# Performance work log

Measured on AMD Instinct MI355X. Metric: run time of the kernel, lower is better.

The kernel has to match this reference:

```python
import jax, jax.numpy as jnp
import numpy as np

N_NODES = 50000
N_EDGES = 600000
D = 128


def _mean_agg(h, src, dst, n_nodes):
    # DGL SAGEConv 'mean': mean of incoming src features per dst node; 0 for isolated nodes
    s = jax.ops.segment_sum(h[src], dst, num_segments=n_nodes)  # [N, d]
    deg = jax.ops.segment_sum(jnp.ones_like(dst, dtype=h.dtype), dst, num_segments=n_nodes)
    return s / jnp.maximum(deg, 1.0)[:, None]


def setup_inputs() -> dict:
    key = jax.random.key(0)
    ks = jax.random.split(key, 10)
    sc = 1.0 / np.sqrt(D)
    return {
        "x": jax.random.normal(ks[0], (N_NODES, D), jnp.float32),
        "e": jax.random.normal(ks[1], (N_EDGES, D), jnp.float32),
        "src": jax.random.randint(ks[2], (N_EDGES,), 0, N_NODES, jnp.int32),
        "dst": jax.random.randint(ks[3], (N_EDGES,), 0, N_NODES, jnp.int32),
        "W1_self": jax.random.normal(ks[4], (D, D), jnp.float32) * sc,
        "W1_neigh": jax.random.normal(ks[5], (D, D), jnp.float32) * sc,
        "b1": jnp.zeros((D,), jnp.float32),
        "W2_self": jax.random.normal(ks[6], (D, D), jnp.float32) * sc,
        "W2_neigh": jax.random.normal(ks[7], (D, D), jnp.float32) * sc,
        "b2": jnp.zeros((D,), jnp.float32),
        "Wp": jax.random.normal(ks[8], (2 * D, 3), jnp.float32) * (1.0 / np.sqrt(2 * D)),
        "bp": jnp.zeros((3,), jnp.float32),
    }


def reference(x, e, src, dst, W1_self, W1_neigh, b1, W2_self, W2_neigh, b2, Wp, bp):
    n = x.shape[0]
    # SAGEConv 1 (mean) + ReLU
    agg1 = _mean_agg(x, src, dst, n)
    h = jax.nn.relu(x @ W1_self + agg1 @ W1_neigh + b1)
    # SAGEConv 2 (mean)
    agg2 = _mean_agg(h, src, dst, n)
    h = h @ W2_self + agg2 @ W2_neigh + b2
    # MLPPredictor: per-edge gather, concat, linear (edge feature e unused in score)
    he = jnp.concatenate([h[src], h[dst]], axis=1)  # [E, 2D]
    score = he @ Wp + bp  # [E, 3]
    return score
```

## Files before the change

### kernel.cpp

```cpp
#include <hip/hip_runtime.h>
#include <hip/hip_bf16.h>


typedef __attribute__((ext_vector_type(8))) short bf16x8;
typedef __attribute__((ext_vector_type(4))) float f32x4;
typedef __attribute__((ext_vector_type(2))) float f32x2;

#if defined(__has_builtin)
#if __has_builtin(__builtin_amdgcn_cvt_pk_f32_fp8)
#define USE_FP8_GATHER 1
#endif
#endif
#ifndef USE_FP8_GATHER
#define USE_FP8_GATHER 0
#endif

static __device__ __forceinline__ float bf16lo(unsigned u) {
    return __uint_as_float(u << 16);
}
static __device__ __forceinline__ float bf16hi(unsigned u) {
    return __uint_as_float(u & 0xffff0000u);
}
static __device__ __forceinline__ unsigned short f2bf(float f) {
    unsigned u = __float_as_uint(f);
    unsigned r = 0x7fffu + ((u >> 16) & 1u);
    return (unsigned short)((u + r) >> 16);
}
static __device__ __forceinline__ unsigned pack_bf162(float a, float b) {
    return (unsigned)f2bf(a) | ((unsigned)f2bf(b) << 16);
}

static __device__ __forceinline__ unsigned f2fp8(float f) {
    unsigned b = __float_as_uint(f);
    unsigned s = (b >> 24) & 0x80u;
    float af = fabsf(f);
    unsigned code;
    if (af < 0.015625f) {
        code = (unsigned)rintf(af * 512.f);
    } else {
        unsigned u = (b & 0x7FFFFFFFu) + 0x7FFFFu + ((b >> 20) & 1u);
        unsigned e = (u >> 23) - 120u;
        code = (e << 3) | ((u >> 20) & 7u);
    }
    return s | code;
}

#define SORT_BLOCKS 128

__global__ __launch_bounds__(256) void k_misc(
    const float* __restrict__ x, unsigned short* __restrict__ xb,
    unsigned char* __restrict__ xq,
    const int* __restrict__ dst, int* __restrict__ H,
    const float* __restrict__ W1s, const float* __restrict__ W1n,
    unsigned short* __restrict__ Wt1,
    const float* __restrict__ W2s, const float* __restrict__ W2n,
    const float* __restrict__ Wp, const float* __restrict__ b2,
    const float* __restrict__ bp, float* __restrict__ Wc,
    float* __restrict__ bconst, int N, int E, int CHUNK)
{
    const int nCvt = (N * 32 + 255) / 256;
    const int b = blockIdx.x;
    const int t = threadIdx.x;

    if (b < nCvt) {
        int i = b * 256 + t;
        if (i < N * 32) {
            float4 v = ((const float4*)x)[i];
            uint2 o;
            o.x = pack_bf162(v.x, v.y);
            o.y = pack_bf162(v.z, v.w);
            *(uint2*)(xb + (size_t)i * 4) = o;
            unsigned q = f2fp8(v.x) | (f2fp8(v.y) << 8) |
                         (f2fp8(v.z) << 16) | (f2fp8(v.w) << 24);
            *(unsigned*)(xq + (size_t)i * 4) = q;
        }
    } else if (b < nCvt + SORT_BLOCKS) {
        __shared__ int hist[256];
        hist[t] = 0;
        __syncthreads();
        int blk = b - nCvt;
        int start = blk * CHUNK;
        int end = min(start + CHUNK, E);
        for (int e = start + t; e < end; e += 256)
            atomicAdd(&hist[((unsigned)dst[e]) >> 8], 1);
        __syncthreads();
        H[blk * 256 + t] = hist[t];
    } else if (b < nCvt + SORT_BLOCKS + 128) {
        int id = (b - nCvt - SORT_BLOCKS) * 256 + t;
        int k = id >> 7, n = id & 127;
        float v;
        if (k < 128) {
            v = W1s[k * 128 + n];
        } else {
#if USE_FP8_GATHER
            int K = k - 128;
            int ksb = K >> 5, r = K & 31, lkp = r >> 3, i = r & 7;
            int orig = lkp * 32 + ksb * 8 + i;
            v = W1n[orig * 128 + n];
#else
            v = W1n[(k - 128) * 128 + n];
#endif
        }
        Wt1[n * 256 + k] = f2bf(v);
    } else {
        for (int id = t; id < 1539; id += 256) {
            if (id < 1536) {
                int c = id / 12, j = id % 12;
                int q = j / 3, jj = j % 3;
                const float* W2 = (q == 0 || q == 2) ? W2s : W2n;
                int wpoff = (q < 2) ? 0 : 128;
                float s = 0.f;
                for (int m = 0; m < 128; ++m)
                    s += W2[c * 128 + m] * Wp[(wpoff + m) * 3 + jj];
                Wc[c * 12 + j] = s;
            } else {
                int jj = id - 1536;
                float s = bp[jj];
                for (int m = 0; m < 128; ++m)
                    s += b2[m] * (Wp[m * 3 + jj] + Wp[(128 + m) * 3 + jj]);
                bconst[jj] = s;
            }
        }
    }
}

__global__ __launch_bounds__(256) void k_s3(const int* __restrict__ src,
                                            const int* __restrict__ dst,
                                            const int* __restrict__ H,
                                            int* __restrict__ packed,
                                            int* __restrict__ bucketBase,
                                            int E, int CHUNK) {
    __shared__ int lt[256];
    __shared__ int cur[256];
    const int t = threadIdx.x, blk = blockIdx.x;
    int tot = 0, pre = 0;
    for (int b = 0; b < SORT_BLOCKS; ++b) {
        int h = H[b * 256 + t];
        pre += (b < blk) ? h : 0;
        tot += h;
    }
    lt[t] = tot;
    __syncthreads();
    for (int off = 1; off < 256; off <<= 1) {
        int u = (t >= off) ? lt[t - off] : 0;
        __syncthreads();
        lt[t] += u;
        __syncthreads();
    }
    int excl = lt[t] - tot;
    cur[t] = excl + pre;
    if (blk == 0) {
        bucketBase[t] = excl;
        if (t == 0) bucketBase[256] = E;
    }
    __syncthreads();
    int start = blk * CHUNK, end = min(start + CHUNK, E);
    for (int e = start + t; e < end; e += 256) {
        int d = dst[e];
        int p = atomicAdd(&cur[((unsigned)d) >> 8], 1);
        packed[p] = (src[e] & 0xFFFF) | ((d & 255) << 16);
    }
}

__global__ __launch_bounds__(256) void k_s4(const int* __restrict__ packed,
                                            const int* __restrict__ bucketBase,
                                            int* __restrict__ eidx,
                                            int* __restrict__ cursor,
                                            float* __restrict__ fdeg,
                                            float* __restrict__ invdeg, int N) {
    const int t = threadIdx.x, b = blockIdx.x;
    const int rb = bucketBase[b], re = bucketBase[b + 1];
    __shared__ int cnt[256];
    __shared__ int lt[256];
    __shared__ int cur[256];
    cnt[t] = 0;
    __syncthreads();
    for (int i = rb + t; i < re; i += 256)
        atomicAdd(&cnt[(packed[i] >> 16) & 255], 1);
    __syncthreads();
    int v = cnt[t];
    lt[t] = v;
    __syncthreads();
    for (int off = 1; off < 256; off <<= 1) {
        int u = (t >= off) ? lt[t - off] : 0;
        __syncthreads();
        lt[t] += u;
        __syncthreads();
    }
    int excl = lt[t] - v;
    int node = b * 256 + t;
    if (node < N) {
        cursor[node] = rb + excl + v;
        fdeg[node] = (float)v;
        invdeg[node] = 1.0f / fmaxf((float)v, 1.0f);
    }
    cur[t] = rb + excl;
    __syncthreads();
    for (int i = rb + t; i < re; i += 256) {
        int p = packed[i];
        int pos = atomicAdd(&cur[(p >> 16) & 255], 1);
        eidx[pos] = p & 0xFFFF;
    }
}

__global__ __launch_bounds__(256) void k_gemm_fused(
    const unsigned short* __restrict__ xb,
    const unsigned char* __restrict__ xq,
    const int* __restrict__ eidx, const int* __restrict__ cursor,
    const float* __restrict__ fdeg, const float* __restrict__ invdeg,
    const unsigned short* __restrict__ Wt, const float* __restrict__ bias,
    const float* __restrict__ Wc, float* __restrict__ P, int N)
{
    __shared__ __align__(16) char sW[65536];
    __shared__ float sWc[1536];
    const int t = threadIdx.x;
    const int wave = t >> 6, lane = t & 63;
    const int lrow = lane & 15, lk = lane >> 4;
    const int r0 = blockIdx.x * 64 + wave * 16 + lrow;

    int* eidxL = (int*)sW;
    const int nb0 = blockIdx.x * 64;
    const int lastN = min(nb0 + 63, N - 1);
    const int estart = cursor[nb0] - (int)fdeg[nb0];
    const int eend = cursor[lastN];
    const int ecnt = eend - estart;
    const bool ldsOK = (ecnt <= 16384);
    if (ldsOK) {
        for (int i = t; i < ecnt; i += 256) eidxL[i] = eidx[estart + i];
    }
    __syncthreads();

    union { bf16x8 v; unsigned u[4]; } afrag0[4];

#if USE_FP8_GATHER
#define ACCQ(AGG, A, B)                                                      \
    {                                                                        \
        f32x2 p;                                                             \
        p = __builtin_amdgcn_cvt_pk_f32_fp8((int)(A).x, false);              \
        AGG[0][0] += p.x; AGG[0][1] += p.y;                                  \
        p = __builtin_amdgcn_cvt_pk_f32_fp8((int)(A).x, true);               \
        AGG[0][2] += p.x; AGG[0][3] += p.y;                                  \
        p = __builtin_amdgcn_cvt_pk_f32_fp8((int)(A).y, false);              \
        AGG[0][4] += p.x; AGG[0][5] += p.y;                                  \
        p = __builtin_amdgcn_cvt_pk_f32_fp8((int)(A).y, true);               \
        AGG[0][6] += p.x; AGG[0][7] += p.y;                                  \
        p = __builtin_amdgcn_cvt_pk_f32_fp8((int)(A).z, false);              \
        AGG[1][0] += p.x; AGG[1][1] += p.y;                                  \
        p = __builtin_amdgcn_cvt_pk_f32_fp8((int)(A).z, true);               \
        AGG[1][2] += p.x; AGG[1][3] += p.y;                                  \
        p = __builtin_amdgcn_cvt_pk_f32_fp8((int)(A).w, false);              \
        AGG[1][4] += p.x; AGG[1][5] += p.y;                                  \
        p = __builtin_amdgcn_cvt_pk_f32_fp8((int)(A).w, true);               \
        AGG[1][6] += p.x; AGG[1][7] += p.y;                                  \
        p = __builtin_amdgcn_cvt_pk_f32_fp8((int)(B).x, false);              \
        AGG[2][0] += p.x; AGG[2][1] += p.y;                                  \
        p = __builtin_amdgcn_cvt_pk_f32_fp8((int)(B).x, true);               \
        AGG[2][2] += p.x; AGG[2][3] += p.y;                                  \
        p = __builtin_amdgcn_cvt_pk_f32_fp8((int)(B).y, false);              \
        AGG[2][4] += p.x; AGG[2][5] += p.y;                                  \
        p = __builtin_amdgcn_cvt_pk_f32_fp8((int)(B).y, true);               \
        AGG[2][6] += p.x; AGG[2][7] += p.y;                                  \
        p = __builtin_amdgcn_cvt_pk_f32_fp8((int)(B).z, false);              \
        AGG[3][0] += p.x; AGG[3][1] += p.y;                                  \
        p = __builtin_amdgcn_cvt_pk_f32_fp8((int)(B).z, true);               \
        AGG[3][2] += p.x; AGG[3][3] += p.y;                                  \
        p = __builtin_amdgcn_cvt_pk_f32_fp8((int)(B).w, false);              \
        AGG[3][4] += p.x; AGG[3][5] += p.y;                                  \
        p = __builtin_amdgcn_cvt_pk_f32_fp8((int)(B).w, true);               \
        AGG[3][6] += p.x; AGG[3][7] += p.y;                                  \
    }
#endif

    {
        float agg[4][8];
#pragma unroll
        for (int k = 0; k < 4; ++k)
#pragma unroll
            for (int i = 0; i < 8; ++i) agg[k][i] = 0.f;

        if (r0 < N) {
            int d = (int)fdeg[r0];
            int o;
            const int* EP;
            if (ldsOK) { EP = eidxL; o = cursor[r0] - d - estart; }
            else       { EP = eidx;  o = cursor[r0] - d; }
            int j = 0;
#if USE_FP8_GATHER
            for (; j + 2 <= d; j += 2) {
                int s0 = EP[o + j], s1 = EP[o + j + 1];
                const unsigned char* row0 = xq + (size_t)s0 * 128 + lk * 32;
                const unsigned char* row1 = xq + (size_t)s1 * 128 + lk * 32;
                uint4 A0 = *(const uint4*)(row0);
                uint4 B0 = *(const uint4*)(row0 + 16);
                uint4 A1 = *(const uint4*)(row1);
                uint4 B1 = *(const uint4*)(row1 + 16);
                ACCQ(agg, A0, B0)
                ACCQ(agg, A1, B1)
            }
            if (j < d) {
                int s0 = EP[o + j];
                const unsigned char* row0 = xq + (size_t)s0 * 128 + lk * 32;
                uint4 A0 = *(const uint4*)(row0);
                uint4 B0 = *(const uint4*)(row0 + 16);
                ACCQ(agg, A0, B0)
            }
#else
            for (; j + 2 <= d; j += 2) {
                int s0 = EP[o + j], s1 = EP[o + j + 1];
                const unsigned short* row0 = xb + (size_t)s0 * 128 + lk * 8;
                const unsigned short* row1 = xb + (size_t)s1 * 128 + lk * 8;
                uint4 v0[4], v1[4];
#pragma unroll
                for (int k = 0; k < 4; ++k) {
                    v0[k] = *(const uint4*)(row0 + k * 32);
                    v1[k] = *(const uint4*)(row1 + k * 32);
                }
#pragma unroll
                for (int k = 0; k < 4; ++k) {
                    agg[k][0] += bf16lo(v0[k].x); agg[k][1] += bf16hi(v0[k].x);
                    agg[k][2] += bf16lo(v0[k].y); agg[k][3] += bf16hi(v0[k].y);
                    agg[k][4] += bf16lo(v0[k].z); agg[k][5] += bf16hi(v0[k].z);
                    agg[k][6] += bf16lo(v0[k].w); agg[k][7] += bf16hi(v0[k].w);
                    agg[k][0] += bf16lo(v1[k].x); agg[k][1] += bf16hi(v1[k].x);
                    agg[k][2] += bf16lo(v1[k].y); agg[k][3] += bf16hi(v1[k].y);
                    agg[k][4] += bf16lo(v1[k].z); agg[k][5] += bf16hi(v1[k].z);
                    agg[k][6] += bf16lo(v1[k].w); agg[k][7] += bf16hi(v1[k].w);
                }
            }
            if (j < d) {
                int s0 = EP[o + j];
                const unsigned short* row0 = xb + (size_t)s0 * 128 + lk * 8;
#pragma unroll
                for (int k = 0; k < 4; ++k) {
                    uint4 v0 = *(const uint4*)(row0 + k * 32);
                    agg[k][0] += bf16lo(v0.x); agg[k][1] += bf16hi(v0.x);
                    agg[k][2] += bf16lo(v0.y); agg[k][3] += bf16hi(v0.y);
                    agg[k][4] += bf16lo(v0.z); agg[k][5] += bf16hi(v0.z);
                    agg[k][6] += bf16lo(v0.w); agg[k][7] += bf16hi(v0.w);
                }
            }
#endif
            float sc = invdeg[r0];
#pragma unroll
            for (int k = 0; k < 4; ++k)
#pragma unroll
                for (int i = 0; i < 4; ++i)
                    afrag0[k].u[i] = pack_bf162(agg[k][2 * i] * sc,
                                                agg[k][2 * i + 1] * sc);
        } else {
#pragma unroll
            for (int k = 0; k < 4; ++k)
#pragma unroll
                for (int i = 0; i < 4; ++i) afrag0[k].u[i] = 0u;
        }
    }

    __syncthreads();
#pragma unroll
    for (int i = 0; i < 16; ++i) {
        int o = (i * 256 + t) * 16;
        int n = o >> 9;
        int c = o & 511;
        int sw = (n << 9) | (c ^ ((n & 7) << 4));
        *(float4*)&sW[sw] = *(const float4*)((const char*)Wt + o);
    }
    for (int i = t; i < 1536; i += 256) sWc[i] = Wc[i];

    f32x4 acc[8];
#pragma unroll
    for (int nb = 0; nb < 8; ++nb) acc[nb] = (f32x4){0.f, 0.f, 0.f, 0.f};

    __syncthreads();

    for (int ks = 0; ks < 8; ++ks) {
        bf16x8 a0;
        if (ks < 4) {
            const int kk = ks * 32 + lk * 8;
            a0 = (bf16x8){};
            if (r0 < N) a0 = *(const bf16x8*)(xb + (size_t)r0 * 128 + kk);
        } else {
            a0 = afrag0[ks - 4].v;
        }
        const int cbase = ks * 64 + lk * 16;
#pragma unroll
        for (int nb = 0; nb < 8; ++nb) {
            int n = nb * 16 + lrow;
            int sw = (n << 9) | (cbase ^ ((n & 7) << 4));
            bf16x8 b = *(const bf16x8*)&sW[sw];
            acc[nb] = __builtin_amdgcn_mfma_f32_16x16x32_bf16(a0, b, acc[nb], 0, 0, 0);
        }
    }

    {
        float hval[8][4];
#pragma unroll
        for (int nb = 0; nb < 8; ++nb) {
            float bv = bias[nb * 16 + lrow];
#pragma unroll
            for (int r = 0; r < 4; ++r)
                hval[nb][r] = fmaxf(acc[nb][r] + bv, 0.f);
        }
#pragma unroll
        for (int r = 0; r < 4; ++r) {
            float pj[12];
#pragma unroll
            for (int j = 0; j < 12; ++j) pj[j] = 0.f;
#pragma unroll
            for (int nb = 0; nb < 8; ++nb) {
                float hv = hval[nb][r];
                const float* wrow = &sWc[(nb * 16 + lrow) * 12];
#pragma unroll
                for (int j = 0; j < 12; ++j) pj[j] += hv * wrow[j];
            }
#pragma unroll
            for (int off = 8; off; off >>= 1) {
#pragma unroll
                for (int j = 0; j < 12; ++j) pj[j] += __shfl_xor(pj[j], off, 64);
            }
            int node = blockIdx.x * 64 + wave * 16 + lk * 4 + r;
            if (lrow == 0 && node < N) {
                float* prow = &P[(size_t)node * 16];
                *(float4*)(prow + 0)  = make_float4(pj[0], pj[1], pj[2], pj[6]);
                *(float4*)(prow + 4)  = make_float4(pj[7], pj[8], 0.f, 0.f);
                *(float4*)(prow + 8)  = make_float4(pj[3], pj[4], pj[5], pj[9]);
                *(float4*)(prow + 12) = make_float4(pj[10], pj[11], 0.f, 0.f);
            }
        }
    }
}

__global__ __launch_bounds__(256) void k_agg3(const float* __restrict__ P,
                                              const int* __restrict__ eidx,
                                              const int* __restrict__ cursor,
                                              const float* __restrict__ fdeg,
                                              const float* __restrict__ invdeg,
                                              float4* __restrict__ ps4,
                                              float4* __restrict__ pd4, int N) {
    int g = blockIdx.x * 256 + threadIdx.x;
    if (g >= N) return;
    int d = (int)fdeg[g];
    int o = cursor[g] - d;
    float a0 = 0.f, a1 = 0.f, a2 = 0.f, a3 = 0.f, a4 = 0.f, a5 = 0.f;
    int i = 0;
    for (; i + 2 <= d; i += 2) {
        int s0 = eidx[o + i], s1 = eidx[o + i + 1];
        float4 u0 = *(const float4*)&P[(size_t)s0 * 16 + 8];
        float4 u1 = *(const float4*)&P[(size_t)s0 * 16 + 12];
        float4 w0 = *(const float4*)&P[(size_t)s1 * 16 + 8];
        float4 w1 = *(const float4*)&P[(size_t)s1 * 16 + 12];
        a0 += u0.x; a1 += u0.y; a2 += u0.z; a3 += u0.w; a4 += u1.x; a5 += u1.y;
        a0 += w0.x; a1 += w0.y; a2 += w0.z; a3 += w0.w; a4 += w1.x; a5 += w1.y;
    }
    if (i < d) {
        int s0 = eidx[o + i];
        float4 u0 = *(const float4*)&P[(size_t)s0 * 16 + 8];
        float4 u1 = *(const float4*)&P[(size_t)s0 * 16 + 12];
        a0 += u0.x; a1 += u0.y; a2 += u0.z; a3 += u0.w; a4 += u1.x; a5 += u1.y;
    }
    float sc = invdeg[g];
    float4 s0v = *(const float4*)&P[(size_t)g * 16];
    float4 s1v = *(const float4*)&P[(size_t)g * 16 + 4];
    ps4[g] = make_float4(s0v.x + a0 * sc, s0v.y + a1 * sc, s0v.z + a2 * sc, 0.f);
    pd4[g] = make_float4(s0v.w + a3 * sc, s1v.x + a4 * sc, s1v.y + a5 * sc, 0.f);
}

__global__ void k_edge(const float4* __restrict__ ps4, const float4* __restrict__ pd4,
                       const int* __restrict__ src, const int* __restrict__ dst,
                       const float* __restrict__ bconst, float* __restrict__ out, int E)
{
    int e = blockIdx.x * blockDim.x + threadIdx.x;
    if (e >= E) return;
    float4 a = ps4[src[e]];
    float4 b = pd4[dst[e]];
    out[(size_t)e * 3 + 0] = a.x + b.x + bconst[0];
    out[(size_t)e * 3 + 1] = a.y + b.y + bconst[1];
    out[(size_t)e * 3 + 2] = a.z + b.z + bconst[2];
}

extern "C" void kernel_launch(void* const* d_in, const int* in_sizes, int n_in,
                              void* d_out, int out_size, void* d_ws, size_t ws_size,
                              hipStream_t stream)
{
    const float* x   = (const float*)d_in[0];
    const int*   src = (const int*)d_in[2];
    const int*   dst = (const int*)d_in[3];
    const float* W1s = (const float*)d_in[4];
    const float* W1n = (const float*)d_in[5];
    const float* b1  = (const float*)d_in[6];
    const float* W2s = (const float*)d_in[7];
    const float* W2n = (const float*)d_in[8];
    const float* b2  = (const float*)d_in[9];
    const float* Wp  = (const float*)d_in[10];
    const float* bp  = (const float*)d_in[11];
    const int N = in_sizes[0] / 128;
    const int E = in_sizes[2];
    float* out = (float*)d_out;

    const int NB = (N + 255) / 256;
    const int CHUNK = (E + SORT_BLOCKS - 1) / SORT_BLOCKS;

    char* wsp = (char*)d_ws;
    auto alloc = [&](size_t bytes) { char* p = wsp; wsp += (bytes + 255) & ~(size_t)255; return p; };
    float* fdeg     = (float*)alloc((size_t)N * 4);
    float* invdeg   = (float*)alloc((size_t)N * 4);
    int*   cursor   = (int*)alloc((size_t)N * 4);
    int*   eidx     = (int*)alloc((size_t)E * 4);
    int*   packed   = (int*)alloc((size_t)E * 4);
    int*   H        = (int*)alloc((size_t)SORT_BLOCKS * 256 * 4);
    int*   bucketBase = (int*)alloc(260 * 4);
    unsigned short* xb  = (unsigned short*)alloc((size_t)N * 128 * 2);
    unsigned char*  xq  = (unsigned char*)alloc((size_t)N * 128);
    unsigned short* Wt1 = (unsigned short*)alloc(256 * 128 * 2);
    float* Wc     = (float*)alloc(1536 * 4);
    float* bconst = (float*)alloc(256);
    float* P      = (float*)alloc((size_t)N * 16 * 4);
    float* ps4    = (float*)alloc((size_t)N * 16);
    float* pd4    = (float*)alloc((size_t)N * 16);

    const int nCvt = (N * 32 + 255) / 256;
    k_misc<<<nCvt + SORT_BLOCKS + 129, 256, 0, stream>>>(
        x, xb, xq, dst, H, W1s, W1n, Wt1, W2s, W2n, Wp, b2, bp, Wc, bconst,
        N, E, CHUNK);

    k_s3<<<SORT_BLOCKS, 256, 0, stream>>>(src, dst, H, packed, bucketBase, E, CHUNK);
    k_s4<<<NB, 256, 0, stream>>>(packed, bucketBase, eidx, cursor, fdeg, invdeg, N);

    k_gemm_fused<<<(N + 63) / 64, 256, 0, stream>>>(xb, xq, eidx, cursor,
                                                    fdeg, invdeg,
                                                    Wt1, b1, Wc, P, N);

    k_agg3<<<(N + 255) / 256, 256, 0, stream>>>(P, eidx, cursor, fdeg, invdeg,
                                                (float4*)ps4, (float4*)pd4, N);

    k_edge<<<(E + 255) / 256, 256, 0, stream>>>((const float4*)ps4, (const float4*)pd4,
                                                src, dst, bconst, out, E);
}
```

Before: 155.3 us.

## Fuse all pipeline stages into one cooperative persistent kernel with grid syncs

Replaces the six separate launches (convert/histogram, scatter, bucket sort, fused GEMM, aggregation, edge scoring) with a single cooperative kernel. Stages are separated by grid.sync() and run as grid-stride loops over a persistent grid sized to occupancy, with W1 loaded into LDS once per block instead of once per tile. The aim is to remove launch gaps and per-block weight reloads. In exchange it adds grid-wide barriers, lower occupancy from a large shared-memory footprint, and an LDS edge-index cache that only holds 1024 entries, so dense tiles fall back to global reads. The old multi-kernel path is kept as a fallback if the cooperative launch fails.

```diff
diff --git a/kernel.cpp b/kernel.cpp
--- a/kernel.cpp
+++ b/kernel.cpp
@@ -1,5 +1,8 @@
 #include <hip/hip_runtime.h>
 #include <hip/hip_bf16.h>
+#include <hip/hip_cooperative_groups.h>
+
+namespace cg = cooperative_groups;
 
 
 typedef __attribute__((ext_vector_type(8))) short bf16x8;
@@ -46,191 +49,6 @@
 }
 
 #define SORT_BLOCKS 128
-
-__global__ __launch_bounds__(256) void k_misc(
-    const float* __restrict__ x, unsigned short* __restrict__ xb,
-    unsigned char* __restrict__ xq,
-    const int* __restrict__ dst, int* __restrict__ H,
-    const float* __restrict__ W1s, const float* __restrict__ W1n,
-    unsigned short* __restrict__ Wt1,
-    const float* __restrict__ W2s, const float* __restrict__ W2n,
-    const float* __restrict__ Wp, const float* __restrict__ b2,
-    const float* __restrict__ bp, float* __restrict__ Wc,
-    float* __restrict__ bconst, int N, int E, int CHUNK)
-{
-    const int nCvt = (N * 32 + 255) / 256;
-    const int b = blockIdx.x;
-    const int t = threadIdx.x;
-
-    if (b < nCvt) {
-        int i = b * 256 + t;
-        if (i < N * 32) {
-            float4 v = ((const float4*)x)[i];
-            uint2 o;
-            o.x = pack_bf162(v.x, v.y);
-            o.y = pack_bf162(v.z, v.w);
-            *(uint2*)(xb + (size_t)i * 4) = o;
-            unsigned q = f2fp8(v.x) | (f2fp8(v.y) << 8) |
-                         (f2fp8(v.z) << 16) | (f2fp8(v.w) << 24);
-            *(unsigned*)(xq + (size_t)i * 4) = q;
-        }
-    } else if (b < nCvt + SORT_BLOCKS) {
-        __shared__ int hist[256];
-        hist[t] = 0;
-        __syncthreads();
-        int blk = b - nCvt;
-        int start = blk * CHUNK;
-        int end = min(start + CHUNK, E);
-        for (int e = start + t; e < end; e += 256)
-            atomicAdd(&hist[((unsigned)dst[e]) >> 8], 1);
-        __syncthreads();
-        H[blk * 256 + t] = hist[t];
-    } else if (b < nCvt + SORT_BLOCKS + 128) {
-        int id = (b - nCvt - SORT_BLOCKS) * 256 + t;
-        int k = id >> 7, n = id & 127;
-        float v;
-        if (k < 128) {
-            v = W1s[k * 128 + n];
-        } else {
-#if USE_FP8_GATHER
-            int K = k - 128;
-            int ksb = K >> 5, r = K & 31, lkp = r >> 3, i = r & 7;
-            int orig = lkp * 32 + ksb * 8 + i;
-            v = W1n[orig * 128 + n];
-#else
-            v = W1n[(k - 128) * 128 + n];
-#endif
-        }
-        Wt1[n * 256 + k] = f2bf(v);
-    } else {
-        for (int id = t; id < 1539; id += 256) {
-            if (id < 1536) {
-                int c = id / 12, j = id % 12;
-                int q = j / 3, jj = j % 3;
-                const float* W2 = (q == 0 || q == 2) ? W2s : W2n;
-                int wpoff = (q < 2) ? 0 : 128;
-                float s = 0.f;
-                for (int m = 0; m < 128; ++m)
-                    s += W2[c * 128 + m] * Wp[(wpoff + m) * 3 + jj];
-                Wc[c * 12 + j] = s;
-            } else {
-                int jj = id - 1536;
-                float s = bp[jj];
-                for (int m = 0; m < 128; ++m)
-                    s += b2[m] * (Wp[m * 3 + jj] + Wp[(128 + m) * 3 + jj]);
-                bconst[jj] = s;
-            }
-        }
-    }
-}
-
-__global__ __launch_bounds__(256) void k_s3(const int* __restrict__ src,
-                                            const int* __restrict__ dst,
-                                            const int* __restrict__ H,
-                                            int* __restrict__ packed,
-                                            int* __restrict__ bucketBase,
-                                            int E, int CHUNK) {
-    __shared__ int lt[256];
-    __shared__ int cur[256];
-    const int t = threadIdx.x, blk = blockIdx.x;
-    int tot = 0, pre = 0;
-    for (int b = 0; b < SORT_BLOCKS; ++b) {
-        int h = H[b * 256 + t];
-        pre += (b < blk) ? h : 0;
-        tot += h;
-    }
-    lt[t] = tot;
-    __syncthreads();
-    for (int off = 1; off < 256; off <<= 1) {
-        int u = (t >= off) ? lt[t - off] : 0;
-        __syncthreads();
-        lt[t] += u;
-        __syncthreads();
-    }
-    int excl = lt[t] - tot;
-    cur[t] = excl + pre;
-    if (blk == 0) {
-        bucketBase[t] = excl;
-        if (t == 0) bucketBase[256] = E;
-    }
-    __syncthreads();
-    int start = blk * CHUNK, end = min(start + CHUNK, E);
-    for (int e = start + t; e < end; e += 256) {
-        int d = dst[e];
-        int p = atomicAdd(&cur[((unsigned)d) >> 8], 1);
-        packed[p] = (src[e] & 0xFFFF) | ((d & 255) << 16);
-    }
-}
-
-__global__ __launch_bounds__(256) void k_s4(const int* __restrict__ packed,
-                                            const int* __restrict__ bucketBase,
-                                            int* __restrict__ eidx,
-                                            int* __restrict__ cursor,
-                                            float* __restrict__ fdeg,
-                                            float* __restrict__ invdeg, int N) {
-    const int t = threadIdx.x, b = blockIdx.x;
-    const int rb = bucketBase[b], re = bucketBase[b + 1];
-    __shared__ int cnt[256];
-    __shared__ int lt[256];
-    __shared__ int cur[256];
-    cnt[t] = 0;
-    __syncthreads();
-    for (int i = rb + t; i < re; i += 256)
-        atomicAdd(&cnt[(packed[i] >> 16) & 255], 1);
-    __syncthreads();
-    int v = cnt[t];
-    lt[t] = v;
-    __syncthreads();
-    for (int off = 1; off < 256; off <<= 1) {
-        int u = (t >= off) ? lt[t - off] : 0;
-        __syncthreads();
-        lt[t] += u;
-        __syncthreads();
-    }
-    int excl = lt[t] - v;
-    int node = b * 256 + t;
-    if (node < N) {
-        cursor[node] = rb + excl + v;
-        fdeg[node] = (float)v;
-        invdeg[node] = 1.0f / fmaxf((float)v, 1.0f);
-    }
-    cur[t] = rb + excl;
-    __syncthreads();
-    for (int i = rb + t; i < re; i += 256) {
-        int p = packed[i];
-        int pos = atomicAdd(&cur[(p >> 16) & 255], 1);
-        eidx[pos] = p & 0xFFFF;
-    }
-}
-
-__global__ __launch_bounds__(256) void k_gemm_fused(
-    const unsigned short* __restrict__ xb,
-    const unsigned char* __restrict__ xq,
-    const int* __restrict__ eidx, const int* __restrict__ cursor,
-    const float* __restrict__ fdeg, const float* __restrict__ invdeg,
-    const unsigned short* __restrict__ Wt, const float* __restrict__ bias,
-    const float* __restrict__ Wc, float* __restrict__ P, int N)
-{
-    __shared__ __align__(16) char sW[65536];
-    __shared__ float sWc[1536];
-    const int t = threadIdx.x;
-    const int wave = t >> 6, lane = t & 63;
-    const int lrow = lane & 15, lk = lane >> 4;
-    const int r0 = blockIdx.x * 64 + wave * 16 + lrow;
-
-    int* eidxL = (int*)sW;
-    const int nb0 = blockIdx.x * 64;
-    const int lastN = min(nb0 + 63, N - 1);
-    const int estart = cursor[nb0] - (int)fdeg[nb0];
-    const int eend = cursor[lastN];
-    const int ecnt = eend - estart;
-    const bool ldsOK = (ecnt <= 16384);
-    if (ldsOK) {
-        for (int i = t; i < ecnt; i += 256) eidxL[i] = eidx[estart + i];
-    }
-    __syncthreads();
-
-    union { bf16x8 v; unsigned u[4]; } afrag0[4];
 
 #if USE_FP8_GATHER
 #define ACCQ(AGG, A, B)                                                      \
@@ -271,6 +89,569 @@
     }
 #endif
 
+__global__ __launch_bounds__(256) void k_mega(
+    const float* __restrict__ x, unsigned short* __restrict__ xb,
+    unsigned char* __restrict__ xq,
+    const int* __restrict__ src, const int* __restrict__ dst,
+    int* __restrict__ H, int* __restrict__ packed, int* __restrict__ bucketBase,
+    int* __restrict__ eidx, int* __restrict__ cursor,
+    float* __restrict__ fdeg, float* __restrict__ invdeg,
+    const float* __restrict__ W1s, const float* __restrict__ W1n,
+    unsigned short* __restrict__ Wt1,
+    const float* __restrict__ W2s, const float* __restrict__ W2n,
+    const float* __restrict__ Wp, const float* __restrict__ b2,
+    const float* __restrict__ bp, float* __restrict__ Wc,
+    float* __restrict__ bconst, const float* __restrict__ b1,
+    float* __restrict__ P, float* __restrict__ ps4, float* __restrict__ pd4,
+    float* __restrict__ out, int N, int E, int CHUNK, int NB)
+{
+    cg::grid_group grid = cg::this_grid();
+    __shared__ __align__(16) char sAll[75776];
+    const int t = threadIdx.x;
+    const int nBk = gridDim.x;
+    const int wave = t >> 6, lane = t & 63;
+    const int lrow = lane & 15, lk = lane >> 4;
+
+    for (int i = blockIdx.x * 256 + t; i < N * 32; i += nBk * 256) {
+        float4 v = ((const float4*)x)[i];
+        uint2 o;
+        o.x = pack_bf162(v.x, v.y);
+        o.y = pack_bf162(v.z, v.w);
+        *(uint2*)(xb + (size_t)i * 4) = o;
+        unsigned q = f2fp8(v.x) | (f2fp8(v.y) << 8) |
+                     (f2fp8(v.z) << 16) | (f2fp8(v.w) << 24);
+        *(unsigned*)(xq + (size_t)i * 4) = q;
+    }
+    {
+        int* hist = (int*)sAll;
+        for (int chunk = blockIdx.x; chunk < SORT_BLOCKS; chunk += nBk) {
+            hist[t] = 0;
+            __syncthreads();
+            int start = chunk * CHUNK, end = min(start + CHUNK, E);
+            for (int e = start + t; e < end; e += 256)
+                atomicAdd(&hist[((unsigned)dst[e]) >> 8], 1);
+            __syncthreads();
+            H[chunk * 256 + t] = hist[t];
+            __syncthreads();
+        }
+    }
+    for (int chunk = blockIdx.x; chunk < 128; chunk += nBk) {
+        int id = chunk * 256 + t;
+        int k = id >> 7, n = id & 127;
+        float v;
+        if (k < 128) {
+            v = W1s[k * 128 + n];
+        } else {
+#if USE_FP8_GATHER
+            int K = k - 128;
+            int ksb = K >> 5, r = K & 31, lkp = r >> 3, i = r & 7;
+            v = W1n[(lkp * 32 + ksb * 8 + i) * 128 + n];
+#else
+            v = W1n[(k - 128) * 128 + n];
+#endif
+        }
+        Wt1[n * 256 + k] = f2bf(v);
+    }
+    if (blockIdx.x == 0) {
+        for (int id = t; id < 1539; id += 256) {
+            if (id < 1536) {
+                int c = id / 12, j = id % 12;
+                int q = j / 3, jj = j % 3;
+                const float* W2 = (q == 0 || q == 2) ? W2s : W2n;
+                int wpoff = (q < 2) ? 0 : 128;
+                float s = 0.f;
+                for (int m = 0; m < 128; ++m)
+                    s += W2[c * 128 + m] * Wp[(wpoff + m) * 3 + jj];
+                Wc[c * 12 + j] = s;
+            } else {
+                int jj = id - 1536;
+                float s = bp[jj];
+                for (int m = 0; m < 128; ++m)
+                    s += b2[m] * (Wp[m * 3 + jj] + Wp[(128 + m) * 3 + jj]);
+                bconst[jj] = s;
+            }
+        }
+    }
+    grid.sync();
+
+    {
+        int* lt = (int*)sAll;
+        int* cur = lt + 256;
+        for (int blk = blockIdx.x; blk < SORT_BLOCKS; blk += nBk) {
+            int tot = 0, pre = 0;
+            for (int b = 0; b < SORT_BLOCKS; ++b) {
+                int h = H[b * 256 + t];
+                pre += (b < blk) ? h : 0;
+                tot += h;
+            }
+            lt[t] = tot;
+            __syncthreads();
+            for (int off = 1; off < 256; off <<= 1) {
+                int u = (t >= off) ? lt[t - off] : 0;
+                __syncthreads();
+                lt[t] += u;
+                __syncthreads();
+            }
+            int excl = lt[t] - tot;
+            cur[t] = excl + pre;
+            if (blk == 0) {
+                bucketBase[t] = excl;
+                if (t == 0) bucketBase[256] = E;
+            }
+            __syncthreads();
+            int start = blk * CHUNK, end = min(start + CHUNK, E);
+            for (int e = start + t; e < end; e += 256) {
+                int d = dst[e];
+                int p = atomicAdd(&cur[((unsigned)d) >> 8], 1);
+                packed[p] = (src[e] & 0xFFFF) | ((d & 255) << 16);
+            }
+            __syncthreads();
+        }
+    }
+    grid.sync();
+
+    {
+        int* cnt = (int*)sAll;
+        int* lt = cnt + 256;
+        int* cur = lt + 256;
+        for (int b = blockIdx.x; b < NB; b += nBk) {
+            const int rb = bucketBase[b], re = bucketBase[b + 1];
+            cnt[t] = 0;
+            __syncthreads();
+            for (int i = rb + t; i < re; i += 256)
+                atomicAdd(&cnt[(packed[i] >> 16) & 255], 1);
+            __syncthreads();
+            int v = cnt[t];
+            lt[t] = v;
+            __syncthreads();
+            for (int off = 1; off < 256; off <<= 1) {
+                int u = (t >= off) ? lt[t - off] : 0;
+                __syncthreads();
+                lt[t] += u;
+                __syncthreads();
+            }
+            int excl = lt[t] - v;
+            int node = b * 256 + t;
+            if (node < N) {
+                cursor[node] = rb + excl + v;
+                fdeg[node] = (float)v;
+                invdeg[node] = 1.0f / fmaxf((float)v, 1.0f);
+            }
+            cur[t] = rb + excl;
+            __syncthreads();
+            for (int i = rb + t; i < re; i += 256) {
+                int p = packed[i];
+                int pos = atomicAdd(&cur[(p >> 16) & 255], 1);
+                eidx[pos] = p & 0xFFFF;
+            }
+            __syncthreads();
+        }
+    }
+    grid.sync();
+
+    {
+        char* sW = sAll;
+        float* sWc = (float*)(sAll + 65536);
+        int* eidxC = (int*)(sAll + 65536 + 6144);
+
+#pragma unroll
+        for (int i = 0; i < 16; ++i) {
+            int o = (i * 256 + t) * 16;
+            int n = o >> 9, c = o & 511;
+            int sw = (n << 9) | (c ^ ((n & 7) << 4));
+            *(float4*)&sW[sw] = *(const float4*)((const char*)Wt1 + o);
+        }
+        for (int i = t; i < 1536; i += 256) sWc[i] = Wc[i];
+        __syncthreads();
+
+        const int nGb = (N + 63) / 64;
+        for (int gb = blockIdx.x; gb < nGb; gb += nBk) {
+            const int nb0 = gb * 64;
+            const int lastN = min(nb0 + 63, N - 1);
+            const int estart = cursor[nb0] - (int)fdeg[nb0];
+            const int eend = cursor[lastN];
+            const int ecnt = eend - estart;
+            const bool ldsOK = (ecnt <= 1024);
+            if (ldsOK) {
+                for (int i = t; i < ecnt; i += 256) eidxC[i] = eidx[estart + i];
+            }
+            __syncthreads();
+
+            const int r0 = nb0 + wave * 16 + lrow;
+            union { bf16x8 v; unsigned u[4]; } afrag0[4];
+            {
+                float agg[4][8];
+#pragma unroll
+                for (int k = 0; k < 4; ++k)
+#pragma unroll
+                    for (int i = 0; i < 8; ++i) agg[k][i] = 0.f;
+
+                if (r0 < N) {
+                    int d = (int)fdeg[r0];
+                    int o;
+                    const int* EP;
+                    if (ldsOK) { EP = eidxC; o = cursor[r0] - d - estart; }
+                    else       { EP = eidx;  o = cursor[r0] - d; }
+                    int j = 0;
+#if USE_FP8_GATHER
+                    for (; j + 2 <= d; j += 2) {
+                        int s0 = EP[o + j], s1 = EP[o + j + 1];
+                        const unsigned char* row0 = xq + (size_t)s0 * 128 + lk * 32;
+                        const unsigned char* row1 = xq + (size_t)s1 * 128 + lk * 32;
+                        uint4 A0 = *(const uint4*)(row0);
+                        uint4 B0 = *(const uint4*)(row0 + 16);
+                        uint4 A1 = *(const uint4*)(row1);
+                        uint4 B1 = *(const uint4*)(row1 + 16);
+                        ACCQ(agg, A0, B0)
+                        ACCQ(agg, A1, B1)
+                    }
+                    if (j < d) {
+                        int s0 = EP[o + j];
+                        const unsigned char* row0 = xq + (size_t)s0 * 128 + lk * 32;
+                        uint4 A0 = *(const uint4*)(row0);
+                        uint4 B0 = *(const uint4*)(row0 + 16);
+                        ACCQ(agg, A0, B0)
+                    }
+#else
+                    for (; j + 2 <= d; j += 2) {
+                        int s0 = EP[o + j], s1 = EP[o + j + 1];
+                        const unsigned short* row0 = xb + (size_t)s0 * 128 + lk * 8;
+                        const unsigned short* row1 = xb + (size_t)s1 * 128 + lk * 8;
+                        uint4 v0[4], v1[4];
+#pragma unroll
+                        for (int k = 0; k < 4; ++k) {
+                            v0[k] = *(const uint4*)(row0 + k * 32);
+                            v1[k] = *(const uint4*)(row1 + k * 32);
+                        }
+#pragma unroll
+                        for (int k = 0; k < 4; ++k) {
+                            agg[k][0] += bf16lo(v0[k].x); agg[k][1] += bf16hi(v0[k].x);
+                            agg[k][2] += bf16lo(v0[k].y); agg[k][3] += bf16hi(v0[k].y);
+                            agg[k][4] += bf16lo(v0[k].z); agg[k][5] += bf16hi(v0[k].z);
+                            agg[k][6] += bf16lo(v0[k].w); agg[k][7] += bf16hi(v0[k].w);
+                            agg[k][0] += bf16lo(v1[k].x); agg[k][1] += bf16hi(v1[k].x);
+                            agg[k][2] += bf16lo(v1[k].y); agg[k][3] += bf16hi(v1[k].y);
+                            agg[k][4] += bf16lo(v1[k].z); agg[k][5] += bf16hi(v1[k].z);
+                            agg[k][6] += bf16lo(v1[k].w); agg[k][7] += bf16hi(v1[k].w);
+                        }
+                    }
+                    if (j < d) {
+                        int s0 = EP[o + j];
+                        const unsigned short* row0 = xb + (size_t)s0 * 128 + lk * 8;
+#pragma unroll
+                        for (int k = 0; k < 4; ++k) {
+                            uint4 v0 = *(const uint4*)(row0 + k * 32);
+                            agg[k][0] += bf16lo(v0.x); agg[k][1] += bf16hi(v0.x);
+                            agg[k][2] += bf16lo(v0.y); agg[k][3] += bf16hi(v0.y);
+                            agg[k][4] += bf16lo(v0.z); agg[k][5] += bf16hi(v0.z);
+                            agg[k][6] += bf16lo(v0.w); agg[k][7] += bf16hi(v0.w);
+                        }
+                    }
+#endif
+                    float sc = invdeg[r0];
+#pragma unroll
+                    for (int k = 0; k < 4; ++k)
+#pragma unroll
+                        for (int i = 0; i < 4; ++i)
+                            afrag0[k].u[i] = pack_bf162(agg[k][2 * i] * sc,
+                                                        agg[k][2 * i + 1] * sc);
+                } else {
+#pragma unroll
+                    for (int k = 0; k < 4; ++k)
+#pragma unroll
+                        for (int i = 0; i < 4; ++i) afrag0[k].u[i] = 0u;
+                }
+            }
+
+            f32x4 acc[8];
+#pragma unroll
+            for (int nb = 0; nb < 8; ++nb) acc[nb] = (f32x4){0.f, 0.f, 0.f, 0.f};
+
+            for (int ks = 0; ks < 8; ++ks) {
+                bf16x8 a0;
+                if (ks < 4) {
+                    const int kk = ks * 32 + lk * 8;
+                    a0 = (bf16x8){};
+                    if (r0 < N) a0 = *(const bf16x8*)(xb + (size_t)r0 * 128 + kk);
+                } else {
+                    a0 = afrag0[ks - 4].v;
+                }
+                const int cbase = ks * 64 + lk * 16;
+#pragma unroll
+                for (int nb = 0; nb < 8; ++nb) {
+                    int n = nb * 16 + lrow;
+                    int sw = (n << 9) | (cbase ^ ((n & 7) << 4));
+                    bf16x8 b = *(const bf16x8*)&sW[sw];
+                    acc[nb] = __builtin_amdgcn_mfma_f32_16x16x32_bf16(a0, b, acc[nb], 0, 0, 0);
+                }
+            }
+
+            {
+                float hval[8][4];
+#pragma unroll
+                for (int nb = 0; nb < 8; ++nb) {
+                    float bv = b1[nb * 16 + lrow];
+#pragma unroll
+                    for (int r = 0; r < 4; ++r)
+                        hval[nb][r] = fmaxf(acc[nb][r] + bv, 0.f);
+                }
+#pragma unroll
+                for (int r = 0; r < 4; ++r) {
+                    float pj[12];
+#pragma unroll
+                    for (int j = 0; j < 12; ++j) pj[j] = 0.f;
+#pragma unroll
+                    for (int nb = 0; nb < 8; ++nb) {
+                        float hv = hval[nb][r];
+                        const float* wrow = &sWc[(nb * 16 + lrow) * 12];
+#pragma unroll
+                        for (int j = 0; j < 12; ++j) pj[j] += hv * wrow[j];
+                    }
+#pragma unroll
+                    for (int off = 8; off; off >>= 1) {
+#pragma unroll
+                        for (int j = 0; j < 12; ++j) pj[j] += __shfl_xor(pj[j], off, 64);
+                    }
+                    int node = nb0 + wave * 16 + lk * 4 + r;
+                    if (lrow == 0 && node < N) {
+                        float* prow = &P[(size_t)node * 16];
+                        *(float4*)(prow + 0)  = make_float4(pj[0], pj[1], pj[2], pj[6]);
+                        *(float4*)(prow + 4)  = make_float4(pj[7], pj[8], 0.f, 0.f);
+                        *(float4*)(prow + 8)  = make_float4(pj[3], pj[4], pj[5], pj[9]);
+                        *(float4*)(prow + 12) = make_float4(pj[10], pj[11], 0.f, 0.f);
+                    }
+                }
+            }
+            __syncthreads();
+        }
+    }
+    grid.sync();
+
+    for (int g = blockIdx.x * 256 + t; g < N; g += nBk * 256) {
+        int d = (int)fdeg[g];
+        int o = cursor[g] - d;
+        float a0 = 0.f, a1 = 0.f, a2 = 0.f, a3 = 0.f, a4 = 0.f, a5 = 0.f;
+        int i = 0;
+        for (; i + 2 <= d; i += 2) {
+            int s0 = eidx[o + i], s1 = eidx[o + i + 1];
+            float4 u0 = *(const float4*)&P[(size_t)s0 * 16 + 8];
+            float4 u1 = *(const float4*)&P[(size_t)s0 * 16 + 12];
+            float4 w0 = *(const float4*)&P[(size_t)s1 * 16 + 8];
+            float4 w1 = *(const float4*)&P[(size_t)s1 * 16 + 12];
+            a0 += u0.x; a1 += u0.y; a2 += u0.z; a3 += u0.w; a4 += u1.x; a5 += u1.y;
+            a0 += w0.x; a1 += w0.y; a2 += w0.z; a3 += w0.w; a4 += w1.x; a5 += w1.y;
+        }
+        if (i < d) {
+            int s0 = eidx[o + i];
+            float4 u0 = *(const float4*)&P[(size_t)s0 * 16 + 8];
+            float4 u1 = *(const float4*)&P[(size_t)s0 * 16 + 12];
+            a0 += u0.x; a1 += u0.y; a2 += u0.z; a3 += u0.w; a4 += u1.x; a5 += u1.y;
+        }
+        float sc = invdeg[g];
+        float4 s0v = *(const float4*)&P[(size_t)g * 16];
+        float4 s1v = *(const float4*)&P[(size_t)g * 16 + 4];
+        ((float4*)ps4)[g] = make_float4(s0v.x + a0 * sc, s0v.y + a1 * sc,
+                                        s0v.z + a2 * sc, 0.f);
+        ((float4*)pd4)[g] = make_float4(s0v.w + a3 * sc, s1v.x + a4 * sc,
+                                        s1v.y + a5 * sc, 0.f);
+    }
+    grid.sync();
+
+    {
+        float bc0 = bconst[0], bc1 = bconst[1], bc2 = bconst[2];
+        for (int e = blockIdx.x * 256 + t; e < E; e += nBk * 256) {
+            float4 a = ((const float4*)ps4)[src[e]];
+            float4 b = ((const float4*)pd4)[dst[e]];
+            out[(size_t)e * 3 + 0] = a.x + b.x + bc0;
+            out[(size_t)e * 3 + 1] = a.y + b.y + bc1;
+            out[(size_t)e * 3 + 2] = a.z + b.z + bc2;
+        }
+    }
+}
+
+__global__ __launch_bounds__(256) void k_misc(
+    const float* __restrict__ x, unsigned short* __restrict__ xb,
+    unsigned char* __restrict__ xq,
+    const int* __restrict__ dst, int* __restrict__ H,
+    const float* __restrict__ W1s, const float* __restrict__ W1n,
+    unsigned short* __restrict__ Wt1,
+    const float* __restrict__ W2s, const float* __restrict__ W2n,
+    const float* __restrict__ Wp, const float* __restrict__ b2,
+    const float* __restrict__ bp, float* __restrict__ Wc,
+    float* __restrict__ bconst, int N, int E, int CHUNK)
+{
+    const int nCvt = (N * 32 + 255) / 256;
+    const int b = blockIdx.x;
+    const int t = threadIdx.x;
+
+    if (b < nCvt) {
+        int i = b * 256 + t;
+        if (i < N * 32) {
+            float4 v = ((const float4*)x)[i];
+            uint2 o;
+            o.x = pack_bf162(v.x, v.y);
+            o.y = pack_bf162(v.z, v.w);
+            *(uint2*)(xb + (size_t)i * 4) = o;
+            unsigned q = f2fp8(v.x) | (f2fp8(v.y) << 8) |
+                         (f2fp8(v.z) << 16) | (f2fp8(v.w) << 24);
+            *(unsigned*)(xq + (size_t)i * 4) = q;
+        }
+    } else if (b < nCvt + SORT_BLOCKS) {
+        __shared__ int hist[256];
+        hist[t] = 0;
+        __syncthreads();
+        int blk = b - nCvt;
+        int start = blk * CHUNK;
+        int end = min(start + CHUNK, E);
+        for (int e = start + t; e < end; e += 256)
+            atomicAdd(&hist[((unsigned)dst[e]) >> 8], 1);
+        __syncthreads();
+        H[blk * 256 + t] = hist[t];
+    } else if (b < nCvt + SORT_BLOCKS + 128) {
+        int id = (b - nCvt - SORT_BLOCKS) * 256 + t;
+        int k = id >> 7, n = id & 127;
+        float v;
+        if (k < 128) {
+            v = W1s[k * 128 + n];
+        } else {
+#if USE_FP8_GATHER
+            int K = k - 128;
+            int ksb = K >> 5, r = K & 31, lkp = r >> 3, i = r & 7;
+            v = W1n[(lkp * 32 + ksb * 8 + i) * 128 + n];
+#else
+            v = W1n[(k - 128) * 128 + n];
+#endif
+        }
+        Wt1[n * 256 + k] = f2bf(v);
+    } else {
+        for (int id = t; id < 1539; id += 256) {
+            if (id < 1536) {
+                int c = id / 12, j = id % 12;
+                int q = j / 3, jj = j % 3;
+                const float* W2 = (q == 0 || q == 2) ? W2s : W2n;
+                int wpoff = (q < 2) ? 0 : 128;
+                float s = 0.f;
+                for (int m = 0; m < 128; ++m)
+                    s += W2[c * 128 + m] * Wp[(wpoff + m) * 3 + jj];
+                Wc[c * 12 + j] = s;
+            } else {
+                int jj = id - 1536;
+                float s = bp[jj];
+                for (int m = 0; m < 128; ++m)
+                    s += b2[m] * (Wp[m * 3 + jj] + Wp[(128 + m) * 3 + jj]);
+                bconst[jj] = s;
+            }
+        }
+    }
+}
+
+__global__ __launch_bounds__(256) void k_s3(const int* __restrict__ src,
+                                            const int* __restrict__ dst,
+                                            const int* __restrict__ H,
+                                            int* __restrict__ packed,
+                                            int* __restrict__ bucketBase,
+                                            int E, int CHUNK) {
+    __shared__ int lt[256];
+    __shared__ int cur[256];
+    const int t = threadIdx.x, blk = blockIdx.x;
+    int tot = 0, pre = 0;
+    for (int b = 0; b < SORT_BLOCKS; ++b) {
+        int h = H[b * 256 + t];
+        pre += (b < blk) ? h : 0;
+        tot += h;
+    }
+    lt[t] = tot;
+    __syncthreads();
+    for (int off = 1; off < 256; off <<= 1) {
+        int u = (t >= off) ? lt[t - off] : 0;
+        __syncthreads();
+        lt[t] += u;
+        __syncthreads();
+    }
+    int excl = lt[t] - tot;
+    cur[t] = excl + pre;
+    if (blk == 0) {
+        bucketBase[t] = excl;
+        if (t == 0) bucketBase[256] = E;
+    }
+    __syncthreads();
+    int start = blk * CHUNK, end = min(start + CHUNK, E);
+    for (int e = start + t; e < end; e += 256) {
+        int d = dst[e];
+        int p = atomicAdd(&cur[((unsigned)d) >> 8], 1);
+        packed[p] = (src[e] & 0xFFFF) | ((d & 255) << 16);
+    }
+}
+
+__global__ __launch_bounds__(256) void k_s4(const int* __restrict__ packed,
+                                            const int* __restrict__ bucketBase,
+                                            int* __restrict__ eidx,
+                                            int* __restrict__ cursor,
+                                            float* __restrict__ fdeg,
+                                            float* __restrict__ invdeg, int N) {
+    const int t = threadIdx.x, b = blockIdx.x;
+    const int rb = bucketBase[b], re = bucketBase[b + 1];
+    __shared__ int cnt[256];
+    __shared__ int lt[256];
+    __shared__ int cur[256];
+    cnt[t] = 0;
+    __syncthreads();
+    for (int i = rb + t; i < re; i += 256)
+        atomicAdd(&cnt[(packed[i] >> 16) & 255], 1);
+    __syncthreads();
+    int v = cnt[t];
+    lt[t] = v;
+    __syncthreads();
+    for (int off = 1; off < 256; off <<= 1) {
+        int u = (t >= off) ? lt[t - off] : 0;
+        __syncthreads();
+        lt[t] += u;
+        __syncthreads();
+    }
+    int excl = lt[t] - v;
+    int node = b * 256 + t;
+    if (node < N) {
+        cursor[node] = rb + excl + v;
+        fdeg[node] = (float)v;
+        invdeg[node] = 1.0f / fmaxf((float)v, 1.0f);
+    }
+    cur[t] = rb + excl;
+    __syncthreads();
+    for (int i = rb + t; i < re; i += 256) {
+        int p = packed[i];
+        int pos = atomicAdd(&cur[(p >> 16) & 255], 1);
+        eidx[pos] = p & 0xFFFF;
+    }
+}
+
+__global__ __launch_bounds__(256) void k_gemm_fused(
+    const unsigned short* __restrict__ xb,
+    const unsigned char* __restrict__ xq,
+    const int* __restrict__ eidx, const int* __restrict__ cursor,
+    const float* __restrict__ fdeg, const float* __restrict__ invdeg,
+    const unsigned short* __restrict__ Wt, const float* __restrict__ bias,
+    const float* __restrict__ Wc, float* __restrict__ P, int N)
+{
+    __shared__ __align__(16) char sW[65536];
+    __shared__ float sWc[1536];
+    const int t = threadIdx.x;
+    const int wave = t >> 6, lane = t & 63;
+    const int lrow = lane & 15, lk = lane >> 4;
+    const int r0 = blockIdx.x * 64 + wave * 16 + lrow;
+
+    int* eidxL = (int*)sW;
+    const int nb0 = blockIdx.x * 64;
+    const int lastN = min(nb0 + 63, N - 1);
+    const int estart = cursor[nb0] - (int)fdeg[nb0];
+    const int eend = cursor[lastN];
+    const int ecnt = eend - estart;
+    const bool ldsOK = (ecnt <= 16384);
+    if (ldsOK) {
+        for (int i = t; i < ecnt; i += 256) eidxL[i] = eidx[estart + i];
+    }
+    __syncthreads();
+
+    union { bf16x8 v; unsigned u[4]; } afrag0[4];
     {
         float agg[4][8];
 #pragma unroll
@@ -492,12 +873,12 @@
     const float* b2  = (const float*)d_in[9];
     const float* Wp  = (const float*)d_in[10];
     const float* bp  = (const float*)d_in[11];
-    const int N = in_sizes[0] / 128;
-    const int E = in_sizes[2];
+    int N = in_sizes[0] / 128;
+    int E = in_sizes[2];
     float* out = (float*)d_out;
 
-    const int NB = (N + 255) / 256;
-    const int CHUNK = (E + SORT_BLOCKS - 1) / SORT_BLOCKS;
+    int NB = (N + 255) / 256;
+    int CHUNK = (E + SORT_BLOCKS - 1) / SORT_BLOCKS;
 
     char* wsp = (char*)d_ws;
     auto alloc = [&](size_t bytes) { char* p = wsp; wsp += (bytes + 255) & ~(size_t)255; return p; };
@@ -517,21 +898,43 @@
     float* ps4    = (float*)alloc((size_t)N * 16);
     float* pd4    = (float*)alloc((size_t)N * 16);
 
+    int dev = 0;
+    (void)hipGetDevice(&dev);
+    int cus = 256;
+    (void)hipDeviceGetAttribute(&cus, hipDeviceAttributeMultiprocessorCount, dev);
+    int maxPerCU = 0;
+    if (hipOccupancyMaxActiveBlocksPerMultiprocessor(
+            &maxPerCU, (const void*)k_mega, 256, 0) != hipSuccess || maxPerCU < 1)
+        maxPerCU = 1;
+    int nGb = (N + 63) / 64;
+    int grid = nGb < maxPerCU * cus ? nGb : maxPerCU * cus;
+
+    void* args[] = {
+        (void*)&x, (void*)&xb, (void*)&xq, (void*)&src, (void*)&dst,
+        (void*)&H, (void*)&packed, (void*)&bucketBase, (void*)&eidx,
+        (void*)&cursor, (void*)&fdeg, (void*)&invdeg,
+        (void*)&W1s, (void*)&W1n, (void*)&Wt1,
+        (void*)&W2s, (void*)&W2n, (void*)&Wp, (void*)&b2, (void*)&bp,
+        (void*)&Wc, (void*)&bconst, (void*)&b1,
+        (void*)&P, (void*)&ps4, (void*)&pd4, (void*)&out,
+        (void*)&N, (void*)&E, (void*)&CHUNK, (void*)&NB
+    };
+
+    hipError_t le = hipLaunchCooperativeKernel((const void*)k_mega,
+                                               dim3(grid), dim3(256),
+                                               args, 0, stream);
+    if (le == hipSuccess) return;
+
     const int nCvt = (N * 32 + 255) / 256;
     k_misc<<<nCvt + SORT_BLOCKS + 129, 256, 0, stream>>>(
         x, xb, xq, dst, H, W1s, W1n, Wt1, W2s, W2n, Wp, b2, bp, Wc, bconst,
         N, E, CHUNK);
-
     k_s3<<<SORT_BLOCKS, 256, 0, stream>>>(src, dst, H, packed, bucketBase, E, CHUNK);
     k_s4<<<NB, 256, 0, stream>>>(packed, bucketBase, eidx, cursor, fdeg, invdeg, N);
-
     k_gemm_fused<<<(N + 63) / 64, 256, 0, stream>>>(xb, xq, eidx, cursor,
-                                                    fdeg, invdeg,
-                                                    Wt1, b1, Wc, P, N);
-
+                                                    fdeg, invdeg, Wt1, b1, Wc, P, N);
     k_agg3<<<(N + 255) / 256, 256, 0, stream>>>(P, eidx, cursor, fdeg, invdeg,
                                                 (float4*)ps4, (float4*)pd4, N);
-
     k_edge<<<(E + 255) / 256, 256, 0, stream>>>((const float4*)ps4, (const float4*)pd4,
                                                 src, dst, bconst, out, E);
 }
```

After: 330.0 us. 2.13x slower.
